# Performance work log

Hardware: AMD Instinct MI355X
Metric: run time of the kernel (lower is better)

The kernel has to match this reference:

```python
import jax, jax.numpy as jnp
import numpy as np

V, NB, NJ, NP, NK = 6890, 10, 24, 207, 19
PARENTS = np.array([-1, 0, 0, 0, 1, 2, 3, 4, 5, 6, 7, 8, 9, 9, 9, 12, 13, 14, 16, 17, 18, 19, 20, 21])


def setup_inputs():
    key = jax.random.key(0)
    ks = jax.random.split(key, 9)
    B = 1024
    beta = jax.random.normal(ks[0], (B, NB), jnp.float32)
    theta = jax.random.normal(ks[1], (B, NJ * 3), jnp.float32) * 0.3  # axis-angle per joint
    trans = jax.random.normal(ks[2], (B, 3), jnp.float32)
    v_template = jax.random.normal(ks[3], (V, 3), jnp.float32)
    shapedirs = jax.random.normal(ks[4], (NB, V * 3), jnp.float32) * 0.03
    Jr = jax.random.uniform(ks[5], (V, NJ), jnp.float32)
    J_regressor = Jr / jnp.sum(Jr, axis=0, keepdims=True)
    posedirs = jax.random.normal(ks[6], (NP, V * 3), jnp.float32) * 0.01
    jr = jax.random.uniform(ks[7], (V, NK), jnp.float32)
    joint_regressor = jr / jnp.sum(jr, axis=0, keepdims=True)
    w = jax.random.uniform(ks[8], (V, NJ), jnp.float32)
    weights = w / jnp.sum(w, axis=1, keepdims=True)  # LBS weights, rows sum to 1
    return dict(beta=beta, theta=theta, trans=trans, v_template=v_template,
                shapedirs=shapedirs, J_regressor=J_regressor, posedirs=posedirs,
                joint_regressor=joint_regressor, weights=weights)


def batch_rodrigues(theta):
    # theta: (N,3) axis-angle -> (N,3,3) rotation matrices via quaternions (HMR-style)
    angle = jnp.linalg.norm(theta + 1e-8, axis=1, keepdims=True)
    half = angle * 0.5
    v = (theta / angle) * jnp.sin(half)
    quat = jnp.concatenate([jnp.cos(half), v], axis=1)
    quat = quat / jnp.linalg.norm(quat, axis=1, keepdims=True)
    w, x, y, z = quat[:, 0], quat[:, 1], quat[:, 2], quat[:, 3]
    rot = jnp.stack([
        1 - 2 * (y * y + z * z), 2 * (x * y - w * z), 2 * (x * z + w * y),
        2 * (x * y + w * z), 1 - 2 * (x * x + z * z), 2 * (y * z - w * x),
        2 * (x * z - w * y), 2 * (y * z + w * x), 1 - 2 * (x * x + y * y)], axis=1)
    return rot.reshape(-1, 3, 3)


def batch_global_rigid_transformation(Rs, J):
    # Rs: (B,24,3,3), J: (B,24,3); rotate_base=True
    B = Rs.shape[0]
    rot_x = jnp.array([[1., 0., 0.], [0., -1., 0.], [0., 0., -1.]], jnp.float32)
    root_R = Rs[:, 0] @ rot_x

    def make_A(R, t):  # (B,3,3),(B,3) -> (B,4,4)
        top = jnp.concatenate([R, t[:, :, None]], axis=2)
        bot = jnp.broadcast_to(jnp.array([0., 0., 0., 1.], jnp.float32), (B, 1, 4))
        return jnp.concatenate([top, bot], axis=1)

    results = [make_A(root_R, J[:, 0])]
    for i in range(1, NJ):  # fixed 24-joint kinematic chain
        t = J[:, i] - J[:, PARENTS[i]]
        results.append(results[PARENTS[i]] @ make_A(Rs[:, i], t))
    res = jnp.stack(results, axis=1)  # (B,24,4,4)
    new_J = res[:, :, :3, 3]
    j_w0 = jnp.concatenate([J, jnp.zeros_like(J[:, :, :1])], axis=2)  # (B,24,4), homo w=0
    init_bone = jnp.einsum('bjrc,bjc->bjr', res, j_w0)
    A = res.at[:, :, :, 3].add(-init_bone)  # subtract only last column (matches F.pad trick)
    return new_J, A


def reference(beta, theta, trans, v_template, shapedirs, J_regressor, posedirs, joint_regressor, weights):
    B = beta.shape[0]
    v_shaped = (beta @ shapedirs).reshape(B, V, 3) + v_template
    J = jnp.einsum('bvc,vj->bjc', v_shaped, J_regressor)  # (B,24,3)
    Rs = batch_rodrigues(theta.reshape(-1, 3)).reshape(B, NJ, 3, 3)
    pose_feature = (Rs[:, 1:] - jnp.eye(3, dtype=Rs.dtype)).reshape(B, NP)
    v_posed = (pose_feature @ posedirs).reshape(B, V, 3) + v_shaped
    _, A = batch_global_rigid_transformation(Rs, J)
    T = jnp.einsum('vj,bjrc->bvrc', weights, A)  # (B,V,4,4) per-vertex skinning transforms
    homo = jnp.concatenate([v_posed, jnp.ones((B, V, 1), v_posed.dtype)], axis=2)
    verts = jnp.einsum('bvrc,bvc->bvr', T, homo)[:, :, :3] + trans[:, None, :]
    joints = jnp.einsum('bvc,vk->bkc', verts, joint_regressor)  # (B,19,3)
    return joints
```

## Files before the change

### kernel.cpp

```cpp
#include <hip/hip_runtime.h>
#include <hip/hip_bf16.h>

constexpr int Vn   = 6890;
constexpr int VC3  = 20670;
constexpr int NKB  = 216;
constexpr int QT   = 224;
constexpr int NMG  = 14;
constexpr int NCOL = 480;
constexpr int MC   = 1368;
constexpr int KCH  = 27;

using bf16x8  = __attribute__((ext_vector_type(8))) short;
using floatx4 = __attribute__((ext_vector_type(4))) float;

__device__ __forceinline__ unsigned short f2bf(float f) {
    unsigned int u = __float_as_uint(f);
    unsigned int r = (u + 0x7FFFu + ((u >> 16) & 1u)) >> 16;
    return (unsigned short)r;
}

__global__ __launch_bounds__(256) void k0_build(
    const float* __restrict__ vt, const float* __restrict__ sdirs,
    const float* __restrict__ pdirs, const float* __restrict__ Jreg,
    const float* __restrict__ jreg, const float* __restrict__ wts,
    unsigned short* __restrict__ Af, unsigned short* __restrict__ Bf)
{
    int bx = blockIdx.x, t = threadIdx.x;
    if (bx < 756) {
        int mg = bx / 54, ub = bx % 54;
        int ql = t & 15, q = mg * 16 + ql;
        int uu = ub * 16 + (t >> 4);
        int v0 = uu * 8, base = 3 * v0;
        float buf[24];
        if (q == 0) {
            #pragma unroll
            for (int i = 0; i < 24; ++i) buf[i] = (v0 + i / 3 < Vn) ? 1.f : 0.f;
        } else {
            const float* src = nullptr;
            if (q == 1) src = vt;
            else if (q >= 2 && q < 12)   src = sdirs + (size_t)(q - 2) * VC3;
            else if (q >= 12 && q < 219) src = pdirs + (size_t)(q - 12) * VC3;
            if (src && base + 23 < VC3) {
                #pragma unroll
                for (int i = 0; i < 12; ++i) {
                    float2 f = *(const float2*)(src + base + 2 * i);
                    buf[2 * i] = f.x; buf[2 * i + 1] = f.y;
                }
            } else {
                #pragma unroll
                for (int i = 0; i < 24; ++i)
                    buf[i] = (src && base + i < VC3) ? src[base + i] : 0.f;
            }
        }
        int kb = uu >> 2, quad = uu & 3;
        size_t foff = (size_t)(ql + quad * 16) * 8;
        #pragma unroll
        for (int c = 0; c < 3; ++c) {
            bf16x8 o;
            #pragma unroll
            for (int j = 0; j < 8; ++j) o[j] = (short)f2bf(buf[3 * j + c]);
            *(bf16x8*)(Af + ((size_t)(c * NMG + mg) * NKB + kb) * 512 + foff) = o;
        }
        return;
    }
    bx -= 756;
    {
        int v0 = bx * 64;
        __shared__ float js[64 * 19], wsh[64 * 24], Jsh[64 * 24];
        for (int i = t; i < 64 * 19; i += 256)
            js[i] = (v0 * 19 + i < Vn * 19) ? jreg[v0 * 19 + i] : 0.f;
        for (int i = t; i < 64 * 24; i += 256) {
            wsh[i] = (v0 * 24 + i < Vn * 24) ? wts[v0 * 24 + i] : 0.f;
            Jsh[i] = (v0 * 24 + i < Vn * 24) ? Jreg[v0 * 24 + i] : 0.f;
        }
        __syncthreads();
        for (int s = t; s < 4096; s += 256) {
            int clow = s & 15, w = s >> 4;
            int vg = w & 7, chigh = w >> 3;
            int col = chigh * 16 + clow;
            int kb = (v0 >> 5) + (vg >> 2);
            bf16x8 o;
            #pragma unroll
            for (int j = 0; j < 8; ++j) {
                int vl = vg * 8 + j;
                float val = 0.f;
                if (col < 456)      val = js[vl * 19 + col / 24] * wsh[vl * 24 + col % 24];
                else if (col < 480) val = Jsh[vl * 24 + (col - 456)];
                o[j] = (short)f2bf(val);
            }
            *(bf16x8*)(Bf + ((size_t)chigh * NKB + kb) * 512
                          + (size_t)(clow + (vg & 3) * 16) * 8) = o;
        }
    }
}

__device__ __forceinline__ void k1_load(bf16x8 (&a)[2], bf16x8 (&b)[4],
    const unsigned short* __restrict__ ap, const unsigned short* __restrict__ bp, int i)
{
    a[0] = *(const bf16x8*)(ap + (size_t)(0 * NKB + i) * 512);
    a[1] = *(const bf16x8*)(ap + (size_t)(1 * NKB + i) * 512);
    b[0] = *(const bf16x8*)(bp + (size_t)(0 * NKB + i) * 512);
    b[1] = *(const bf16x8*)(bp + (size_t)(1 * NKB + i) * 512);
    b[2] = *(const bf16x8*)(bp + (size_t)(2 * NKB + i) * 512);
    b[3] = *(const bf16x8*)(bp + (size_t)(3 * NKB + i) * 512);
}

__global__ __launch_bounds__(512) void k1_mfma(
    const unsigned short* __restrict__ Af, const unsigned short* __restrict__ Bf,
    unsigned short* __restrict__ Wb3, float* __restrict__ w1g,
    float* __restrict__ Jacc)
{
    __shared__ float red[8 * 2048];
    int tid = threadIdx.x;
    int wv = tid >> 6, l = tid & 63;
    int r = blockIdx.x;
    int c = r / 56; r %= 56;
    int mt = r >> 3, nt = r & 7;
    int kb0 = wv * KCH;

    const unsigned short* ap = Af + ((size_t)(c * NMG + mt * 2) * NKB + kb0) * 512 + l * 8;
    const unsigned short* bp = Bf + ((size_t)(nt * 4) * NKB + kb0) * 512 + l * 8;

    floatx4 acc[2][4];
    #pragma unroll
    for (int mi = 0; mi < 2; ++mi)
        #pragma unroll
        for (int ni = 0; ni < 4; ++ni) acc[mi][ni] = floatx4{0.f, 0.f, 0.f, 0.f};

    bf16x8 a[3][2], b[3][4];
    k1_load(a[0], b[0], ap, bp, 0);
    k1_load(a[1], b[1], ap, bp, 1);
    #pragma unroll
    for (int i = 0; i < KCH; ++i) {
        if (i + 2 < KCH) k1_load(a[(i + 2) % 3], b[(i + 2) % 3], ap, bp, i + 2);
        bf16x8 (&ac)[2] = a[i % 3];
        bf16x8 (&bc)[4] = b[i % 3];
        #pragma unroll
        for (int mi = 0; mi < 2; ++mi)
            #pragma unroll
            for (int ni = 0; ni < 4; ++ni)
                acc[mi][ni] = __builtin_amdgcn_mfma_f32_16x16x32_bf16(ac[mi], bc[ni], acc[mi][ni], 0, 0, 0);
    }
    #pragma unroll
    for (int mi = 0; mi < 2; ++mi)
        #pragma unroll
        for (int ni = 0; ni < 4; ++ni)
            *(floatx4*)&red[wv * 2048 + ((mi * 4 + ni) * 64 + l) * 4] = acc[mi][ni];
    __syncthreads();
    if (tid < 256) {
        int cl = tid & 63, qo = tid >> 6;
        int ni = cl >> 4;
        int q0 = qo * 8;
        int li0 = ((q0 & 15) >> 2) * 16 + (cl & 15);
        int li1 = (((q0 + 4) & 15) >> 2) * 16 + (cl & 15);
        int base0 = (((q0 >> 4) * 4 + ni) * 64 + li0) * 4;
        int base1 = ((((q0 + 4) >> 4) * 4 + ni) * 64 + li1) * 4;
        floatx4 s0{0.f, 0.f, 0.f, 0.f}, s1{0.f, 0.f, 0.f, 0.f};
        #pragma unroll
        for (int ww = 0; ww < 8; ++ww) {
            s0 += *(const floatx4*)&red[ww * 2048 + base0];
            s1 += *(const floatx4*)&red[ww * 2048 + base1];
        }
        int col = nt * 64 + cl;
        if (col < NCOL) {
            int colc = col * 3 + c;
            if (colc < MC) {
                bf16x8 o;
                #pragma unroll
                for (int j = 0; j < 4; ++j) {
                    o[j]     = (short)f2bf(s0[j]);
                    o[4 + j] = (short)f2bf(s1[j]);
                }
                *(bf16x8*)(Wb3 + ((size_t)(colc >> 4) * 7 + mt) * 512
                               + (size_t)((colc & 15) + qo * 16) * 8) = o;
            }
            if (c == 0 && mt == 0 && qo == 0 && col < 456) w1g[col] = s0[0];
            if (mt == 0 && col >= 456) {
                float* jb = Jacc + (size_t)((col - 456) * 3 + c) * 11;
                if (qo == 0) {
                    jb[0] = s0[1]; jb[1] = s0[2]; jb[2] = s0[3];
                    jb[3] = s1[0]; jb[4] = s1[1]; jb[5] = s1[2]; jb[6] = s1[3];
                } else if (qo == 1) {
                    jb[7] = s0[0]; jb[8] = s0[1]; jb[9] = s0[2]; jb[10] = s0[3];
                }
            }
        }
    }
}

__global__ __launch_bounds__(256) void k2_fused(
    const unsigned short* __restrict__ Wb3, const float* __restrict__ Jacc,
    const float* __restrict__ w1g, const float* __restrict__ beta,
    const float* __restrict__ theta, const float* __restrict__ trans,
    float* __restrict__ Mg, float* __restrict__ out)
{
    __shared__ float Rs[16][24][9];
    __shared__ float Jl[16][24][3];
    __shared__ float resR[16][24][9];
    __shared__ float rest_[16][24][3];
    __shared__ float tA[16][72];
    __shared__ float bet[16][10];
    __shared__ float w1s[456];
    __shared__ unsigned short xls[7 * 512];
    int t = threadIdx.x;
    int b0 = blockIdx.x * 16;

    if (t < 160) bet[t / 10][t % 10] = beta[(b0 + t / 10) * 10 + t % 10];
    for (int i = t; i < 456; i += 256) w1s[i] = w1g[i];
    for (int i = t; i < 384; i += 256) {
        int bl = i / 24, j = i % 24;
        float t0 = theta[(size_t)(b0 + bl) * 72 + j * 3 + 0];
        float t1 = theta[(size_t)(b0 + bl) * 72 + j * 3 + 1];
        float t2 = theta[(size_t)(b0 + bl) * 72 + j * 3 + 2];
        float e0 = t0 + 1e-8f, e1 = t1 + 1e-8f, e2 = t2 + 1e-8f;
        float angle = sqrtf(e0 * e0 + e1 * e1 + e2 * e2);
        float half = 0.5f * angle;
        float sh = sinf(half), ch = cosf(half);
        float s = sh / angle;
        float qx = t0 * s, qy = t1 * s, qz = t2 * s;
        float qn = sqrtf(ch * ch + qx * qx + qy * qy + qz * qz);
        float w = ch / qn, x = qx / qn, y = qy / qn, z = qz / qn;
        Rs[bl][j][0] = 1.f - 2.f * (y * y + z * z);
        Rs[bl][j][1] = 2.f * (x * y - w * z);
        Rs[bl][j][2] = 2.f * (x * z + w * y);
        Rs[bl][j][3] = 2.f * (x * y + w * z);
        Rs[bl][j][4] = 1.f - 2.f * (x * x + z * z);
        Rs[bl][j][5] = 2.f * (y * z - w * x);
        Rs[bl][j][6] = 2.f * (x * z - w * y);
        Rs[bl][j][7] = 2.f * (y * z + w * x);
        Rs[bl][j][8] = 1.f - 2.f * (x * x + y * y);
    }
    __syncthreads();
    for (int i = t; i < 16 * 72; i += 256) {
        int bl = i / 72, jc = i % 72;
        const float* bp_ = Jacc + (size_t)jc * 11;
        float a = bp_[0];
        #pragma unroll
        for (int n = 0; n < 10; ++n) a += bet[bl][n] * bp_[1 + n];
        Jl[bl][jc / 3][jc % 3] = a;
    }
    for (int i = t; i < 16 * QT; i += 256) {
        int q = i >> 4, bl = i & 15;
        float xv = 0.f;
        if (q == 1) xv = 1.f;
        else if (q >= 2 && q < 12) xv = bet[bl][q - 2];
        else if (q >= 12 && q < 219) {
            int p = q - 12;
            int jj = 1 + p / 9, e = p % 9;
            float rr = Rs[bl][jj][e];
            if (e == 0 || e == 4 || e == 8) rr -= 1.f;
            xv = rr;
        }
        xls[(size_t)(q >> 5) * 512 + (size_t)(bl + ((q >> 3) & 3) * 16) * 8 + (q & 7)]
            = f2bf(xv);
    }
    __syncthreads();
    {
        int l = t & 63, wv = t >> 6;
        bf16x8 xb[7];
        #pragma unroll
        for (int kk = 0; kk < 7; ++kk)
            xb[kk] = *(const bf16x8*)(xls + (size_t)kk * 512 + l * 8);
        for (int mg = wv; mg < 86; mg += 4) {
            const unsigned short* apg = Wb3 + (size_t)mg * 7 * 512 + l * 8;
            floatx4 acc{0.f, 0.f, 0.f, 0.f};
            #pragma unroll
            for (int kk = 0; kk < 7; ++kk)
                acc = __builtin_amdgcn_mfma_f32_16x16x32_bf16(
                    *(const bf16x8*)(apg + (size_t)kk * 512), xb[kk], acc, 0, 0, 0);
            int bl = l & 15, cc0 = mg * 16 + (l >> 4) * 4;
            if (cc0 < MC)
                *(floatx4*)(Mg + (size_t)(b0 + bl) * MC + cc0) = acc;
        }
    }
    if (t < 48) {
        const int par[24] = {-1,0,0,0,1,2,3,4,5,6,7,8,9,9,9,12,13,14,16,17,18,19,20,21};
        int bl = t / 3, rr = t % 3;
        resR[bl][0][rr * 3 + 0] =  Rs[bl][0][rr * 3 + 0];
        resR[bl][0][rr * 3 + 1] = -Rs[bl][0][rr * 3 + 1];
        resR[bl][0][rr * 3 + 2] = -Rs[bl][0][rr * 3 + 2];
        rest_[bl][0][rr] = Jl[bl][0][rr];
        for (int i = 1; i < 24; ++i) {
            int p = par[i];
            float t0 = Jl[bl][i][0] - Jl[bl][p][0];
            float t1 = Jl[bl][i][1] - Jl[bl][p][1];
            float t2 = Jl[bl][i][2] - Jl[bl][p][2];
            float a0 = resR[bl][p][rr * 3 + 0], a1 = resR[bl][p][rr * 3 + 1],
                  a2 = resR[bl][p][rr * 3 + 2];
            resR[bl][i][rr * 3 + 0] = a0 * Rs[bl][i][0] + a1 * Rs[bl][i][3] + a2 * Rs[bl][i][6];
            resR[bl][i][rr * 3 + 1] = a0 * Rs[bl][i][1] + a1 * Rs[bl][i][4] + a2 * Rs[bl][i][7];
            resR[bl][i][rr * 3 + 2] = a0 * Rs[bl][i][2] + a1 * Rs[bl][i][5] + a2 * Rs[bl][i][8];
            rest_[bl][i][rr] = a0 * t0 + a1 * t1 + a2 * t2 + rest_[bl][p][rr];
        }
    }
    __syncthreads();
    for (int i = t; i < 16 * 72; i += 256) {
        int bl = i / 72, jc = i % 72;
        int j = jc / 3, c = jc % 3;
        tA[bl][jc] = rest_[bl][j][c]
            - (resR[bl][j][c * 3 + 0] * Jl[bl][j][0] + resR[bl][j][c * 3 + 1] * Jl[bl][j][1]
             + resR[bl][j][c * 3 + 2] * Jl[bl][j][2]);
    }
    __syncthreads();
    for (int i = t; i < 16 * 57; i += 256) {
        int lb = i / 57, kc = i % 57;
        int k = kc / 3, c = kc % 3;
        int b = b0 + lb;
        float acc = trans[b * 3 + c];
        const float* Mrow = Mg + (size_t)b * MC;
        #pragma unroll
        for (int j = 0; j < 24; ++j) {
            int kj = k * 24 + j;
            float m0 = Mrow[kj * 3 + 0], m1 = Mrow[kj * 3 + 1], m2 = Mrow[kj * 3 + 2];
            acc += resR[lb][j][c * 3 + 0] * m0
                 + resR[lb][j][c * 3 + 1] * m1
                 + resR[lb][j][c * 3 + 2] * m2
                 + tA[lb][j * 3 + c] * w1s[kj];
        }
        out[b * 57 + kc] = acc;
    }
}

extern "C" void kernel_launch(void* const* d_in, const int* in_sizes, int n_in,
                              void* d_out, int out_size, void* d_ws, size_t ws_size,
                              hipStream_t stream)
{
    const float* beta  = (const float*)d_in[0];
    const float* theta = (const float*)d_in[1];
    const float* trans = (const float*)d_in[2];
    const float* vt    = (const float*)d_in[3];
    const float* sdirs = (const float*)d_in[4];
    const float* Jreg  = (const float*)d_in[5];
    const float* pdirs = (const float*)d_in[6];
    const float* jreg  = (const float*)d_in[7];
    const float* wts   = (const float*)d_in[8];
    float* out = (float*)d_out;
    int B = in_sizes[0] / 10;

    unsigned short* Af  = (unsigned short*)d_ws;
    unsigned short* Bf  = Af + (size_t)42 * NKB * 512;
    unsigned short* Wb3 = Bf + (size_t)32 * NKB * 512;
    float* Jacc = (float*)(Wb3 + (size_t)88 * 7 * 512);
    float* w1g  = Jacc + 792;
    float* Mg   = w1g + 456;

    k0_build<<<dim3(756 + 108), 256, 0, stream>>>(
        vt, sdirs, pdirs, Jreg, jreg, wts, Af, Bf);
    k1_mfma<<<dim3(168), 512, 0, stream>>>(Af, Bf, Wb3, w1g, Jacc);
    k2_fused<<<dim3(B / 16), 256, 0, stream>>>(
        Wb3, Jacc, w1g, beta, theta, trans, Mg, out);
}
```

Before: 153.4 us.

## Split fused per-batch kernel into prep, tiled MFMA GEMM, and combine kernels

The single k2_fused kernel (64 blocks of 16 batch rows, each re-streaming the whole Wb3 matrix) is replaced by three kernels. A prep kernel builds the bf16 pose/shape feature matrix and the rigid transforms per batch into global buffers. A 2D-tiled MFMA GEMM kernel (176 blocks, each wave computing a 2x4 tile grid) reuses loaded A/B fragments across tiles. A combine kernel stages Mg rows in LDS to produce the joints. The intent is more parallelism across the GPU and less redundant weight traffic, at the cost of two extra launches and global round-trips for the intermediates.

```diff
diff --git a/kernel.cpp b/kernel.cpp
--- a/kernel.cpp
+++ b/kernel.cpp
@@ -188,26 +188,24 @@
     }
 }
 
-__global__ __launch_bounds__(256) void k2_fused(
-    const unsigned short* __restrict__ Wb3, const float* __restrict__ Jacc,
-    const float* __restrict__ w1g, const float* __restrict__ beta,
-    const float* __restrict__ theta, const float* __restrict__ trans,
-    float* __restrict__ Mg, float* __restrict__ out)
-{
-    __shared__ float Rs[16][24][9];
-    __shared__ float Jl[16][24][3];
-    __shared__ float resR[16][24][9];
-    __shared__ float rest_[16][24][3];
-    __shared__ float tA[16][72];
-    __shared__ float bet[16][10];
-    __shared__ float w1s[456];
-    __shared__ unsigned short xls[7 * 512];
+__global__ __launch_bounds__(256) void k2a_prep(
+    const float* __restrict__ Jacc, const float* __restrict__ beta,
+    const float* __restrict__ theta,
+    unsigned short* __restrict__ xbf, float* __restrict__ RAg, float* __restrict__ tAg)
+{
+    __shared__ float Rs[4][24][9];
+    __shared__ float Jl[4][24][3];
+    __shared__ float resR[4][24][9];
+    __shared__ float rest_[4][24][3];
+    __shared__ float bet[4][10];
+    __shared__ float Jas[792];
     int t = threadIdx.x;
-    int b0 = blockIdx.x * 16;
-
-    if (t < 160) bet[t / 10][t % 10] = beta[(b0 + t / 10) * 10 + t % 10];
-    for (int i = t; i < 456; i += 256) w1s[i] = w1g[i];
-    for (int i = t; i < 384; i += 256) {
+    int b0 = blockIdx.x * 4;
+
+    if (t < 40) bet[t / 10][t % 10] = beta[(b0 + t / 10) * 10 + t % 10];
+    for (int i = t; i < 792; i += 256) Jas[i] = Jacc[i];
+    if (t >= 64 && t < 160) {
+        int i = t - 64;
         int bl = i / 24, j = i % 24;
         float t0 = theta[(size_t)(b0 + bl) * 72 + j * 3 + 0];
         float t1 = theta[(size_t)(b0 + bl) * 72 + j * 3 + 1];
@@ -231,16 +229,17 @@
         Rs[bl][j][8] = 1.f - 2.f * (x * x + y * y);
     }
     __syncthreads();
-    for (int i = t; i < 16 * 72; i += 256) {
+    for (int i = t; i < 4 * 72; i += 256) {
         int bl = i / 72, jc = i % 72;
-        const float* bp_ = Jacc + (size_t)jc * 11;
+        const float* bp_ = Jas + (size_t)jc * 11;
         float a = bp_[0];
         #pragma unroll
         for (int n = 0; n < 10; ++n) a += bet[bl][n] * bp_[1 + n];
         Jl[bl][jc / 3][jc % 3] = a;
     }
-    for (int i = t; i < 16 * QT; i += 256) {
-        int q = i >> 4, bl = i & 15;
+    for (int i = t; i < 4 * QT; i += 256) {
+        int q = i >> 2, bl = i & 3;
+        int b = b0 + bl;
         float xv = 0.f;
         if (q == 1) xv = 1.f;
         else if (q >= 2 && q < 12) xv = bet[bl][q - 2];
@@ -251,29 +250,11 @@
             if (e == 0 || e == 4 || e == 8) rr -= 1.f;
             xv = rr;
         }
-        xls[(size_t)(q >> 5) * 512 + (size_t)(bl + ((q >> 3) & 3) * 16) * 8 + (q & 7)]
-            = f2bf(xv);
+        xbf[((size_t)(b >> 4) * 7 + (q >> 5)) * 512
+            + (size_t)((b & 15) + ((q >> 3) & 3) * 16) * 8 + (q & 7)] = f2bf(xv);
     }
     __syncthreads();
-    {
-        int l = t & 63, wv = t >> 6;
-        bf16x8 xb[7];
-        #pragma unroll
-        for (int kk = 0; kk < 7; ++kk)
-            xb[kk] = *(const bf16x8*)(xls + (size_t)kk * 512 + l * 8);
-        for (int mg = wv; mg < 86; mg += 4) {
-            const unsigned short* apg = Wb3 + (size_t)mg * 7 * 512 + l * 8;
-            floatx4 acc{0.f, 0.f, 0.f, 0.f};
-            #pragma unroll
-            for (int kk = 0; kk < 7; ++kk)
-                acc = __builtin_amdgcn_mfma_f32_16x16x32_bf16(
-                    *(const bf16x8*)(apg + (size_t)kk * 512), xb[kk], acc, 0, 0, 0);
-            int bl = l & 15, cc0 = mg * 16 + (l >> 4) * 4;
-            if (cc0 < MC)
-                *(floatx4*)(Mg + (size_t)(b0 + bl) * MC + cc0) = acc;
-        }
-    }
-    if (t < 48) {
+    if (t < 12) {
         const int par[24] = {-1,0,0,0,1,2,3,4,5,6,7,8,9,9,9,12,13,14,16,17,18,19,20,21};
         int bl = t / 3, rr = t % 3;
         resR[bl][0][rr * 3 + 0] =  Rs[bl][0][rr * 3 + 0];
@@ -294,28 +275,98 @@
         }
     }
     __syncthreads();
-    for (int i = t; i < 16 * 72; i += 256) {
+    for (int i = t; i < 4 * 216; i += 256) {
+        int bl = i / 216, jr = i % 216;
+        RAg[(size_t)(b0 + bl) * 216 + jr] = resR[bl][jr / 9][jr % 9];
+    }
+    for (int i = t; i < 4 * 72; i += 256) {
         int bl = i / 72, jc = i % 72;
         int j = jc / 3, c = jc % 3;
-        tA[bl][jc] = rest_[bl][j][c]
+        tAg[(size_t)(b0 + bl) * 72 + jc] = rest_[bl][j][c]
             - (resR[bl][j][c * 3 + 0] * Jl[bl][j][0] + resR[bl][j][c * 3 + 1] * Jl[bl][j][1]
              + resR[bl][j][c * 3 + 2] * Jl[bl][j][2]);
     }
+}
+
+__global__ __launch_bounds__(256) void k2b_mfma(
+    const unsigned short* __restrict__ Wb3, const unsigned short* __restrict__ xbf,
+    float* __restrict__ Mg)
+{
+    int w = threadIdx.x >> 6, l = threadIdx.x & 63;
+    int wm = w & 1, wn = w >> 1;
+    int ct = blockIdx.x % 22, bt = blockIdx.x / 22;
+    int mg0 = ct * 4 + wm * 2;
+    int bg0 = bt * 8 + wn * 4;
+    const unsigned short* ap = Wb3 + (size_t)mg0 * 7 * 512 + l * 8;
+    const unsigned short* bp = xbf + (size_t)bg0 * 7 * 512 + l * 8;
+
+    floatx4 acc[2][4];
+    #pragma unroll
+    for (int mi = 0; mi < 2; ++mi)
+        #pragma unroll
+        for (int ni = 0; ni < 4; ++ni) acc[mi][ni] = floatx4{0.f, 0.f, 0.f, 0.f};
+
+    #pragma unroll
+    for (int kk = 0; kk < 7; ++kk) {
+        bf16x8 a0 = *(const bf16x8*)(ap + (size_t)(0 * 7 + kk) * 512);
+        bf16x8 a1 = *(const bf16x8*)(ap + (size_t)(1 * 7 + kk) * 512);
+        bf16x8 b0 = *(const bf16x8*)(bp + (size_t)(0 * 7 + kk) * 512);
+        bf16x8 b1 = *(const bf16x8*)(bp + (size_t)(1 * 7 + kk) * 512);
+        bf16x8 b2 = *(const bf16x8*)(bp + (size_t)(2 * 7 + kk) * 512);
+        bf16x8 b3 = *(const bf16x8*)(bp + (size_t)(3 * 7 + kk) * 512);
+        acc[0][0] = __builtin_amdgcn_mfma_f32_16x16x32_bf16(a0, b0, acc[0][0], 0, 0, 0);
+        acc[0][1] = __builtin_amdgcn_mfma_f32_16x16x32_bf16(a0, b1, acc[0][1], 0, 0, 0);
+        acc[0][2] = __builtin_amdgcn_mfma_f32_16x16x32_bf16(a0, b2, acc[0][2], 0, 0, 0);
+        acc[0][3] = __builtin_amdgcn_mfma_f32_16x16x32_bf16(a0, b3, acc[0][3], 0, 0, 0);
+        acc[1][0] = __builtin_amdgcn_mfma_f32_16x16x32_bf16(a1, b0, acc[1][0], 0, 0, 0);
+        acc[1][1] = __builtin_amdgcn_mfma_f32_16x16x32_bf16(a1, b1, acc[1][1], 0, 0, 0);
+        acc[1][2] = __builtin_amdgcn_mfma_f32_16x16x32_bf16(a1, b2, acc[1][2], 0, 0, 0);
+        acc[1][3] = __builtin_amdgcn_mfma_f32_16x16x32_bf16(a1, b3, acc[1][3], 0, 0, 0);
+    }
+    int lr = l & 15, rq = (l >> 4) * 4;
+    #pragma unroll
+    for (int mi = 0; mi < 2; ++mi)
+        #pragma unroll
+        for (int ni = 0; ni < 4; ++ni) {
+            int b  = bt * 128 + wn * 64 + ni * 16 + lr;
+            int cc = (mg0 + mi) * 16 + rq;
+            if (cc < MC)
+                *(floatx4*)(Mg + (size_t)b * MC + cc) = acc[mi][ni];
+        }
+}
+
+__global__ __launch_bounds__(256) void k2c_combine(
+    const float* __restrict__ Mg, const float* __restrict__ RAg,
+    const float* __restrict__ tAg, const float* __restrict__ w1g,
+    const float* __restrict__ trans, float* __restrict__ out)
+{
+    __shared__ float w1s[456];
+    __shared__ float Ms[4 * MC];
+    __shared__ float RAs[4 * 216];
+    __shared__ float tAs[4 * 72];
+    int tid = threadIdx.x;
+    int b0 = blockIdx.x * 4;
+    for (int i = tid; i < 456; i += 256) w1s[i] = w1g[i];
+    for (int i = tid; i < 4 * MC; i += 256) Ms[i] = Mg[(size_t)b0 * MC + i];
+    for (int i = tid; i < 4 * 216; i += 256) RAs[i] = RAg[(size_t)b0 * 216 + i];
+    for (int i = tid; i < 4 * 72; i += 256) tAs[i] = tAg[(size_t)b0 * 72 + i];
     __syncthreads();
-    for (int i = t; i < 16 * 57; i += 256) {
-        int lb = i / 57, kc = i % 57;
+    if (tid < 228) {
+        int lb = tid / 57, kc = tid % 57;
         int k = kc / 3, c = kc % 3;
         int b = b0 + lb;
         float acc = trans[b * 3 + c];
-        const float* Mrow = Mg + (size_t)b * MC;
+        const float* Mrow = Ms + lb * MC;
+        const float* RAr  = RAs + lb * 216;
+        const float* tAr  = tAs + lb * 72;
         #pragma unroll
         for (int j = 0; j < 24; ++j) {
             int kj = k * 24 + j;
             float m0 = Mrow[kj * 3 + 0], m1 = Mrow[kj * 3 + 1], m2 = Mrow[kj * 3 + 2];
-            acc += resR[lb][j][c * 3 + 0] * m0
-                 + resR[lb][j][c * 3 + 1] * m1
-                 + resR[lb][j][c * 3 + 2] * m2
-                 + tA[lb][j * 3 + c] * w1s[kj];
+            acc += RAr[j * 9 + c * 3 + 0] * m0
+                 + RAr[j * 9 + c * 3 + 1] * m1
+                 + RAr[j * 9 + c * 3 + 2] * m2
+                 + tAr[j * 3 + c] * w1s[kj];
         }
         out[b * 57 + kc] = acc;
     }
@@ -340,13 +391,18 @@
     unsigned short* Af  = (unsigned short*)d_ws;
     unsigned short* Bf  = Af + (size_t)42 * NKB * 512;
     unsigned short* Wb3 = Bf + (size_t)32 * NKB * 512;
-    float* Jacc = (float*)(Wb3 + (size_t)88 * 7 * 512);
+    unsigned short* xbf = Wb3 + (size_t)88 * 7 * 512;
+    float* Jacc = (float*)(xbf + (size_t)64 * 7 * 512);
     float* w1g  = Jacc + 792;
-    float* Mg   = w1g + 456;
+    float* RAg  = w1g + 456;
+    float* tAg  = RAg + (size_t)B * 216;
+    float* Mg   = tAg + (size_t)B * 72;
 
     k0_build<<<dim3(756 + 108), 256, 0, stream>>>(
         vt, sdirs, pdirs, Jreg, jreg, wts, Af, Bf);
     k1_mfma<<<dim3(168), 512, 0, stream>>>(Af, Bf, Wb3, w1g, Jacc);
-    k2_fused<<<dim3(B / 16), 256, 0, stream>>>(
-        Wb3, Jacc, w1g, beta, theta, trans, Mg, out);
-}
+    k2a_prep<<<dim3(B / 4), 256, 0, stream>>>(
+        Jacc, beta, theta, xbf, RAg, tAg);
+    k2b_mfma<<<dim3((B / 128) * 22), 256, 0, stream>>>(Wb3, xbf, Mg);
+    k2c_combine<<<dim3(B / 4), 256, 0, stream>>>(Mg, RAg, tAg, w1g, trans, out);
+}
```

After: 134.2 us. 12.5% less time.

## Split tail kernel across keypoint groups and keep MFMA results in shared memory

Applied to the files above, without the earlier changes.

The final kernel is split into ten blocks per 16-sample batch tile, each handling two keypoints' worth of MFMA column groups. This raises the block count from 64 to 640. The MFMA output now goes to shared memory instead of a global scratch buffer, so the global write and read-back of Mg is gone. Wave 0 runs the kinematic chain while the other seven waves do the MFMAs. The cost is that Rodrigues, the joint regression and the kinematic chain are recomputed in every one of the ten blocks.

```diff
diff --git a/kernel.cpp b/kernel.cpp
--- a/kernel.cpp
+++ b/kernel.cpp
@@ -188,26 +188,33 @@
     }
 }
 
-__global__ __launch_bounds__(256) void k2_fused(
+__global__ __launch_bounds__(512) void k2_tail(
     const unsigned short* __restrict__ Wb3, const float* __restrict__ Jacc,
     const float* __restrict__ w1g, const float* __restrict__ beta,
     const float* __restrict__ theta, const float* __restrict__ trans,
-    float* __restrict__ Mg, float* __restrict__ out)
+    float* __restrict__ out)
 {
     __shared__ float Rs[16][24][9];
     __shared__ float Jl[16][24][3];
     __shared__ float resR[16][24][9];
     __shared__ float rest_[16][24][3];
-    __shared__ float tA[16][72];
+    __shared__ float tAs[16][72];
     __shared__ float bet[16][10];
+    __shared__ float Jas[792];
     __shared__ float w1s[456];
     __shared__ unsigned short xls[7 * 512];
+    __shared__ float Msh[16][145];
     int t = threadIdx.x;
-    int b0 = blockIdx.x * 16;
+    int bt = blockIdx.x / 10, kp = blockIdx.x % 10;
+    int b0 = bt * 16;
+    int nmg = (kp == 9) ? 5 : 9;
+    int mgbase = kp * 9;
 
     if (t < 160) bet[t / 10][t % 10] = beta[(b0 + t / 10) * 10 + t % 10];
-    for (int i = t; i < 456; i += 256) w1s[i] = w1g[i];
-    for (int i = t; i < 384; i += 256) {
+    for (int i = t; i < 792; i += 512) Jas[i] = Jacc[i];
+    if (t < 456) w1s[t] = w1g[t];
+    if (t >= 128 && t < 512) {
+        int i = t - 128;
         int bl = i / 24, j = i % 24;
         float t0 = theta[(size_t)(b0 + bl) * 72 + j * 3 + 0];
         float t1 = theta[(size_t)(b0 + bl) * 72 + j * 3 + 1];
@@ -231,15 +238,16 @@
         Rs[bl][j][8] = 1.f - 2.f * (x * x + y * y);
     }
     __syncthreads();
-    for (int i = t; i < 16 * 72; i += 256) {
+    for (int i = t; i < 16 * 72; i += 512) {
         int bl = i / 72, jc = i % 72;
-        const float* bp_ = Jacc + (size_t)jc * 11;
+        const float* bp_ = Jas + (size_t)jc * 11;
         float a = bp_[0];
         #pragma unroll
         for (int n = 0; n < 10; ++n) a += bet[bl][n] * bp_[1 + n];
         Jl[bl][jc / 3][jc % 3] = a;
     }
-    for (int i = t; i < 16 * QT; i += 256) {
+    __syncthreads();
+    for (int i = t; i < 16 * QT; i += 512) {
         int q = i >> 4, bl = i & 15;
         float xv = 0.f;
         if (q == 1) xv = 1.f;
@@ -255,69 +263,66 @@
             = f2bf(xv);
     }
     __syncthreads();
-    {
-        int l = t & 63, wv = t >> 6;
-        bf16x8 xb[7];
-        #pragma unroll
-        for (int kk = 0; kk < 7; ++kk)
-            xb[kk] = *(const bf16x8*)(xls + (size_t)kk * 512 + l * 8);
-        for (int mg = wv; mg < 86; mg += 4) {
-            const unsigned short* apg = Wb3 + (size_t)mg * 7 * 512 + l * 8;
+    int wv = t >> 6, l = t & 63;
+    if (wv == 0) {
+        if (t < 48) {
+            const int par[24] = {-1,0,0,0,1,2,3,4,5,6,7,8,9,9,9,12,13,14,16,17,18,19,20,21};
+            int bl = t / 3, rr = t % 3;
+            resR[bl][0][rr * 3 + 0] =  Rs[bl][0][rr * 3 + 0];
+            resR[bl][0][rr * 3 + 1] = -Rs[bl][0][rr * 3 + 1];
+            resR[bl][0][rr * 3 + 2] = -Rs[bl][0][rr * 3 + 2];
+            rest_[bl][0][rr] = Jl[bl][0][rr];
+            for (int i = 1; i < 24; ++i) {
+                int p = par[i];
+                float t0 = Jl[bl][i][0] - Jl[bl][p][0];
+                float t1 = Jl[bl][i][1] - Jl[bl][p][1];
+                float t2 = Jl[bl][i][2] - Jl[bl][p][2];
+                float a0 = resR[bl][p][rr * 3 + 0], a1 = resR[bl][p][rr * 3 + 1],
+                      a2 = resR[bl][p][rr * 3 + 2];
+                resR[bl][i][rr * 3 + 0] = a0 * Rs[bl][i][0] + a1 * Rs[bl][i][3] + a2 * Rs[bl][i][6];
+                resR[bl][i][rr * 3 + 1] = a0 * Rs[bl][i][1] + a1 * Rs[bl][i][4] + a2 * Rs[bl][i][7];
+                resR[bl][i][rr * 3 + 2] = a0 * Rs[bl][i][2] + a1 * Rs[bl][i][5] + a2 * Rs[bl][i][8];
+                rest_[bl][i][rr] = a0 * t0 + a1 * t1 + a2 * t2 + rest_[bl][p][rr];
+            }
+        }
+    } else {
+        for (int mgl = wv - 1; mgl < nmg; mgl += 7) {
+            const unsigned short* ap = Wb3 + (size_t)(mgbase + mgl) * 7 * 512 + l * 8;
             floatx4 acc{0.f, 0.f, 0.f, 0.f};
             #pragma unroll
             for (int kk = 0; kk < 7; ++kk)
                 acc = __builtin_amdgcn_mfma_f32_16x16x32_bf16(
-                    *(const bf16x8*)(apg + (size_t)kk * 512), xb[kk], acc, 0, 0, 0);
-            int bl = l & 15, cc0 = mg * 16 + (l >> 4) * 4;
-            if (cc0 < MC)
-                *(floatx4*)(Mg + (size_t)(b0 + bl) * MC + cc0) = acc;
-        }
-    }
-    if (t < 48) {
-        const int par[24] = {-1,0,0,0,1,2,3,4,5,6,7,8,9,9,9,12,13,14,16,17,18,19,20,21};
-        int bl = t / 3, rr = t % 3;
-        resR[bl][0][rr * 3 + 0] =  Rs[bl][0][rr * 3 + 0];
-        resR[bl][0][rr * 3 + 1] = -Rs[bl][0][rr * 3 + 1];
-        resR[bl][0][rr * 3 + 2] = -Rs[bl][0][rr * 3 + 2];
-        rest_[bl][0][rr] = Jl[bl][0][rr];
-        for (int i = 1; i < 24; ++i) {
-            int p = par[i];
-            float t0 = Jl[bl][i][0] - Jl[bl][p][0];
-            float t1 = Jl[bl][i][1] - Jl[bl][p][1];
-            float t2 = Jl[bl][i][2] - Jl[bl][p][2];
-            float a0 = resR[bl][p][rr * 3 + 0], a1 = resR[bl][p][rr * 3 + 1],
-                  a2 = resR[bl][p][rr * 3 + 2];
-            resR[bl][i][rr * 3 + 0] = a0 * Rs[bl][i][0] + a1 * Rs[bl][i][3] + a2 * Rs[bl][i][6];
-            resR[bl][i][rr * 3 + 1] = a0 * Rs[bl][i][1] + a1 * Rs[bl][i][4] + a2 * Rs[bl][i][7];
-            resR[bl][i][rr * 3 + 2] = a0 * Rs[bl][i][2] + a1 * Rs[bl][i][5] + a2 * Rs[bl][i][8];
-            rest_[bl][i][rr] = a0 * t0 + a1 * t1 + a2 * t2 + rest_[bl][p][rr];
-        }
-    }
-    __syncthreads();
-    for (int i = t; i < 16 * 72; i += 256) {
+                    *(const bf16x8*)(ap + (size_t)kk * 512),
+                    *(const bf16x8*)(xls + (size_t)kk * 512 + l * 8), acc, 0, 0, 0);
+            int bl = l & 15, cc0 = mgl * 16 + (l >> 4) * 4;
+            #pragma unroll
+            for (int rr = 0; rr < 4; ++rr) Msh[bl][cc0 + rr] = acc[rr];
+        }
+    }
+    __syncthreads();
+    for (int i = t; i < 16 * 72; i += 512) {
         int bl = i / 72, jc = i % 72;
         int j = jc / 3, c = jc % 3;
-        tA[bl][jc] = rest_[bl][j][c]
+        tAs[bl][jc] = rest_[bl][j][c]
             - (resR[bl][j][c * 3 + 0] * Jl[bl][j][0] + resR[bl][j][c * 3 + 1] * Jl[bl][j][1]
              + resR[bl][j][c * 3 + 2] * Jl[bl][j][2]);
     }
     __syncthreads();
-    for (int i = t; i < 16 * 57; i += 256) {
-        int lb = i / 57, kc = i % 57;
-        int k = kc / 3, c = kc % 3;
-        int b = b0 + lb;
-        float acc = trans[b * 3 + c];
-        const float* Mrow = Mg + (size_t)b * MC;
+    int nk = (kp == 9) ? 1 : 2;
+    for (int i = t; i < 48 * nk; i += 512) {
+        int kl = i / 48, r2 = i % 48;
+        int bl = r2 / 3, c = r2 % 3;
+        int b = b0 + bl, k = kp * 2 + kl;
+        float s = trans[b * 3 + c];
+        const float* mrow = Msh[bl] + kl * 72;
         #pragma unroll
         for (int j = 0; j < 24; ++j) {
-            int kj = k * 24 + j;
-            float m0 = Mrow[kj * 3 + 0], m1 = Mrow[kj * 3 + 1], m2 = Mrow[kj * 3 + 2];
-            acc += resR[lb][j][c * 3 + 0] * m0
-                 + resR[lb][j][c * 3 + 1] * m1
-                 + resR[lb][j][c * 3 + 2] * m2
-                 + tA[lb][j * 3 + c] * w1s[kj];
-        }
-        out[b * 57 + kc] = acc;
+            s += tAs[bl][j * 3 + c] * w1s[k * 24 + j];
+            s += resR[bl][j][c * 3 + 0] * mrow[j * 3 + 0]
+               + resR[bl][j][c * 3 + 1] * mrow[j * 3 + 1]
+               + resR[bl][j][c * 3 + 2] * mrow[j * 3 + 2];
+        }
+        out[(size_t)b * 57 + k * 3 + c] = s;
     }
 }
 
@@ -342,11 +347,10 @@
     unsigned short* Wb3 = Bf + (size_t)32 * NKB * 512;
     float* Jacc = (float*)(Wb3 + (size_t)88 * 7 * 512);
     float* w1g  = Jacc + 792;
-    float* Mg   = w1g + 456;
 
     k0_build<<<dim3(756 + 108), 256, 0, stream>>>(
         vt, sdirs, pdirs, Jreg, jreg, wts, Af, Bf);
     k1_mfma<<<dim3(168), 512, 0, stream>>>(Af, Bf, Wb3, w1g, Jacc);
-    k2_fused<<<dim3(B / 16), 256, 0, stream>>>(
-        Wb3, Jacc, w1g, beta, theta, trans, Mg, out);
-}
+    k2_tail<<<dim3((B / 16) * 10), 512, 0, stream>>>(
+        Wb3, Jacc, w1g, beta, theta, trans, out);
+}
```

Measured after the change: 130.3 us. -15.0%, faster.
